# Performance work log

Hardware: AMD Instinct MI355X
Metric: run time of the kernel (lower is better)

Reference implementation:

```python
import jax, jax.numpy as jnp
import numpy as np

LN_EPS = 1e-5


def setup_inputs() -> dict:
    key = jax.random.key(0)
    ks = jax.random.split(key, 6)
    N, E, D = 100000, 600000, 128
    x = jax.random.normal(ks[0], (N, D), dtype=jnp.float32)
    edge_index = jax.random.randint(ks[1], (2, E), 0, N, dtype=jnp.int64)
    dropout_mask = jax.random.uniform(ks[2], (N, D), dtype=jnp.float32)
    ln_gamma = jnp.ones((D,), dtype=jnp.float32)
    ln_beta = jnp.zeros((D,), dtype=jnp.float32)
    W_l = jax.random.normal(ks[3], (D, D), dtype=jnp.float32) / np.sqrt(D)
    b_l = jnp.zeros((D,), dtype=jnp.float32)
    W_r = jax.random.normal(ks[4], (D, D), dtype=jnp.float32) / np.sqrt(D)
    return {"x": x, "edge_index": edge_index, "dropout_mask": dropout_mask,
            "ln_gamma": ln_gamma, "ln_beta": ln_beta,
            "W_l": W_l, "b_l": b_l, "W_r": W_r}


def reference(x, edge_index, dropout_mask, ln_gamma, ln_beta, W_l, b_l, W_r):
    N = x.shape[0]
    # LayerNorm (elementwise affine) -> ReLU -> dropout mask
    mu = jnp.mean(x, axis=-1, keepdims=True)
    var = jnp.mean(jnp.square(x - mu), axis=-1, keepdims=True)
    h = (x - mu) * jax.lax.rsqrt(var + LN_EPS) * ln_gamma + ln_beta
    h = jax.nn.relu(h) * dropout_mask  # [N, D]
    # SAGEConv with mean aggregation: messages flow src -> dst
    src, dst = edge_index[0], edge_index[1]
    agg = jax.ops.segment_sum(h[src], dst, num_segments=N)  # [N, D]
    cnt = jax.ops.segment_sum(jnp.ones_like(dst, dtype=h.dtype), dst,
                              num_segments=N)
    mean_agg = agg / jnp.maximum(cnt, 1.0)[:, None]
    # out = lin_l(mean_agg) + lin_r(h); PyG stores weights as [out, in]
    return mean_agg @ W_l.T + b_l + h @ W_r.T
```

## Files before the change

kernel.cpp:

```cpp
#include <hip/hip_runtime.h>

#define LN_EPS 1e-5f
#define D 128
#define SCAN_CHUNK 1024
#define LDSA_STRIDE 264

typedef __attribute__((ext_vector_type(4))) float f32x4;
typedef __attribute__((ext_vector_type(8))) short bf16x8;

static __device__ __forceinline__ ushort f2bf(float f) {
    union { float f; unsigned u; } a; a.f = f;
    unsigned r = a.u + 0x7FFF + ((a.u >> 16) & 1);
    return (ushort)(r >> 16);
}
static __device__ __forceinline__ float bf2f(ushort u) {
    union { unsigned u; float f; } a; a.u = ((unsigned)u) << 16;
    return a.f;
}

__global__ void prep_w(const float* __restrict__ Wl,
                       const float* __restrict__ Wr,
                       ushort* __restrict__ Bfrag) {
    int t = blockIdx.x * blockDim.x + threadIdx.x;
    if (t >= 8 * 8 * 64 * 8) return;
    int i    = t & 7;
    int lane = (t >> 3) & 63;
    int jb   = (t >> 9) & 7;
    int ks   = t >> 12;
    int k = ks * 32 + (lane >> 4) * 8 + i;
    int j = jb * 16 + (lane & 15);
    float v = (k < D) ? Wl[j * D + k] : Wr[j * D + (k - D)];
    Bfrag[t] = f2bf(v);
}

__global__ void ln_relu_drop(const float* __restrict__ x,
                             const float* __restrict__ mask,
                             const float* __restrict__ gamma,
                             const float* __restrict__ beta,
                             ushort* __restrict__ hbf, int N) {
    int node = (blockIdx.x * blockDim.x + threadIdx.x) >> 6;
    int lane = threadIdx.x & 63;
    if (node >= N) return;
    float2 v = ((const float2*)(x + (size_t)node * D))[lane];
    float s  = v.x + v.y;
    float ss = v.x * v.x + v.y * v.y;
#pragma unroll
    for (int off = 32; off > 0; off >>= 1) {
        s  += __shfl_xor(s, off);
        ss += __shfl_xor(ss, off);
    }
    float mu  = s * (1.0f / D);
    float var = ss * (1.0f / D) - mu * mu;
    float rs  = rsqrtf(var + LN_EPS);
    float2 g = ((const float2*)gamma)[lane];
    float2 b = ((const float2*)beta)[lane];
    float2 m = ((const float2*)(mask + (size_t)node * D))[lane];
    ushort2 o;
    o.x = f2bf(fmaxf((v.x - mu) * rs * g.x + b.x, 0.0f) * m.x);
    o.y = f2bf(fmaxf((v.y - mu) * rs * g.y + b.y, 0.0f) * m.y);
    ((ushort2*)(hbf + (size_t)node * D))[lane] = o;
}

__global__ void hist_k(const int* __restrict__ ei, int* __restrict__ hist, int E) {
    int e = blockIdx.x * blockDim.x + threadIdx.x;
    if (e >= E) return;
    atomicAdd(&hist[ei[E + e]], 1);
}

__global__ void scan1(const int* __restrict__ hist, int* __restrict__ offs,
                      int* __restrict__ chunk_sums, int N) {
    __shared__ int lds[256];
    int base = blockIdx.x * SCAN_CHUNK;
    int t = threadIdx.x;
    int idx0 = base + t * 4;
    int v[4];
#pragma unroll
    for (int i = 0; i < 4; i++) {
        int idx = idx0 + i;
        v[i] = (idx < N) ? hist[idx] : 0;
    }
    lds[t] = v[0] + v[1] + v[2] + v[3];
    __syncthreads();
    for (int off = 1; off < 256; off <<= 1) {
        int add = (t >= off) ? lds[t - off] : 0;
        __syncthreads();
        lds[t] += add;
        __syncthreads();
    }
    int run = (t == 0) ? 0 : lds[t - 1];
    if (t == 255) chunk_sums[blockIdx.x] = lds[255];
#pragma unroll
    for (int i = 0; i < 4; i++) {
        int idx = idx0 + i;
        if (idx < N) offs[idx] = run;
        run += v[i];
    }
}

__global__ void scan2(int* __restrict__ chunk_sums, int C) {
    __shared__ int lds[128];
    int t = threadIdx.x;
    lds[t] = (t < C) ? chunk_sums[t] : 0;
    __syncthreads();
    for (int off = 1; off < 128; off <<= 1) {
        int add = (t >= off) ? lds[t - off] : 0;
        __syncthreads();
        lds[t] += add;
        __syncthreads();
    }
    int excl = (t == 0) ? 0 : lds[t - 1];
    if (t < C) chunk_sums[t] = excl;
}

__global__ void scan3(int* __restrict__ offs, const int* __restrict__ chunk_sums,
                      int* __restrict__ cursor, int N) {
    int i = blockIdx.x * blockDim.x + threadIdx.x;
    if (i >= N) return;
    int v = offs[i] + chunk_sums[i / SCAN_CHUNK];
    offs[i] = v;
    cursor[i] = v;
}

__global__ void sort_edges(const int* __restrict__ ei, int* __restrict__ cursor,
                           int* __restrict__ sorted_src, int E) {
    int e = blockIdx.x * blockDim.x + threadIdx.x;
    if (e >= E) return;
    int dst = ei[E + e];
    int pos = atomicAdd(&cursor[dst], 1);
    sorted_src[pos] = ei[e];
}

__global__ void aggregate4(const ushort* __restrict__ hbf,
                           const int* __restrict__ sorted_src,
                           const int* __restrict__ offs,
                           const int* __restrict__ hist,
                           ushort* __restrict__ magg, int N) {
    int wid  = (blockIdx.x * blockDim.x + threadIdx.x) >> 6;
    int lane = threadIdx.x & 63;
    int g  = lane >> 4;
    int sl = lane & 15;
    int node = wid * 4 + g;
    bool valid = node < N;
    int start = 0, deg = 0;
    if (valid) { start = offs[node]; deg = hist[node]; }
    float acc[8];
#pragma unroll
    for (int j = 0; j < 8; j++) acc[j] = 0.0f;
    for (int i = 0; ; i++) {
        bool act = (i < deg);
        if (!__any(act)) break;
        if (act) {
            int src = sorted_src[start + i];
            bf16x8 v = *(const bf16x8*)(hbf + (size_t)src * D + sl * 8);
#pragma unroll
            for (int j = 0; j < 8; j++) acc[j] += bf2f((ushort)v[j]);
        }
    }
    if (valid) {
        float inv = 1.0f / fmaxf((float)deg, 1.0f);
        bf16x8 o;
#pragma unroll
        for (int j = 0; j < 8; j++) o[j] = (short)f2bf(acc[j] * inv);
        *(bf16x8*)(magg + (size_t)node * D + sl * 8) = o;
    }
}

__global__ void __launch_bounds__(256, 3)
out_gemm_mfma(float* __restrict__ out,
              const ushort* __restrict__ magg,
              const ushort* __restrict__ hbf,
              const ushort* __restrict__ Bfrag,
              const float* __restrict__ bl,
              int N) {
    __shared__ ushort Alds[64 * LDSA_STRIDE];
    int tid  = threadIdx.x;
    int wave = tid >> 6;
    int lane = tid & 63;
    int n0 = blockIdx.x * 64;

    bf16x8 breg[8][2];
#pragma unroll
    for (int ks = 0; ks < 8; ks++)
#pragma unroll
        for (int jj = 0; jj < 2; jj++) {
            int jb = wave * 2 + jj;
            breg[ks][jj] = *(const bf16x8*)(Bfrag + (size_t)((ks * 8 + jb) * 64 + lane) * 8);
        }

#pragma unroll
    for (int it = 0; it < 4; it++) {
        int chunk = tid + 256 * it;
        int row = chunk >> 4;
        int c8  = chunk & 15;
        int node = n0 + row;
        bf16x8 va = (bf16x8){0,0,0,0,0,0,0,0};
        bf16x8 vh = (bf16x8){0,0,0,0,0,0,0,0};
        if (node < N) {
            va = *(const bf16x8*)(magg + (size_t)node * D + c8 * 8);
            vh = *(const bf16x8*)(hbf  + (size_t)node * D + c8 * 8);
        }
        *(bf16x8*)&Alds[row * LDSA_STRIDE + c8 * 8]       = va;
        *(bf16x8*)&Alds[row * LDSA_STRIDE + 128 + c8 * 8] = vh;
    }
    __syncthreads();

    f32x4 acc[4][2];
#pragma unroll
    for (int nb = 0; nb < 4; nb++)
#pragma unroll
        for (int jj = 0; jj < 2; jj++)
            acc[nb][jj] = (f32x4){0.f, 0.f, 0.f, 0.f};

    int arow = lane & 15;
    int akoff = (lane >> 4) * 8;
#pragma unroll
    for (int ks = 0; ks < 8; ks++) {
#pragma unroll
        for (int nb = 0; nb < 4; nb++) {
            bf16x8 a = *(const bf16x8*)&Alds[(nb * 16 + arow) * LDSA_STRIDE + ks * 32 + akoff];
            acc[nb][0] = __builtin_amdgcn_mfma_f32_16x16x32_bf16(a, breg[ks][0], acc[nb][0], 0, 0, 0);
            acc[nb][1] = __builtin_amdgcn_mfma_f32_16x16x32_bf16(a, breg[ks][1], acc[nb][1], 0, 0, 0);
        }
    }

    float bias0 = bl[wave * 32 + (lane & 15)];
    float bias1 = bl[wave * 32 + 16 + (lane & 15)];
    int rbase = (lane >> 4) * 4;
#pragma unroll
    for (int nb = 0; nb < 4; nb++) {
#pragma unroll
        for (int r = 0; r < 4; r++) {
            int row = nb * 16 + rbase + r;
            if (n0 + row < N) {
                float* orow = out + (size_t)(n0 + row) * D + wave * 32 + (lane & 15);
                orow[0]  = acc[nb][0][r] + bias0;
                orow[16] = acc[nb][1][r] + bias1;
            }
        }
    }
}

extern "C" void kernel_launch(void* const* d_in, const int* in_sizes, int n_in,
                              void* d_out, int out_size, void* d_ws, size_t ws_size,
                              hipStream_t stream) {
    const float* x     = (const float*)d_in[0];
    const int*   ei    = (const int*)  d_in[1];
    const float* mask  = (const float*)d_in[2];
    const float* gamma = (const float*)d_in[3];
    const float* beta  = (const float*)d_in[4];
    const float* Wl    = (const float*)d_in[5];
    const float* bl    = (const float*)d_in[6];
    const float* Wr    = (const float*)d_in[7];
    float* out = (float*)d_out;

    int N = in_sizes[0] / D;
    int E = in_sizes[1] / 2;
    int chunks = (N + SCAN_CHUNK - 1) / SCAN_CHUNK;

    ushort* hbf   = (ushort*)d_ws;
    ushort* magg  = hbf + (size_t)N * D;
    ushort* Bfrag = magg + (size_t)N * D;
    int* hist   = (int*)(Bfrag + 32768);
    int* offs   = hist + N;
    int* cursor = offs + N;
    int* csums  = cursor + N;
    int* ssrc   = csums + 128;

    hipMemsetAsync(hist, 0, (size_t)N * sizeof(int), stream);
    prep_w<<<128, 256, 0, stream>>>(Wl, Wr, Bfrag);
    ln_relu_drop<<<(N + 3) / 4, 256, 0, stream>>>(x, mask, gamma, beta, hbf, N);
    hist_k<<<(E + 255) / 256, 256, 0, stream>>>(ei, hist, E);
    scan1<<<chunks, 256, 0, stream>>>(hist, offs, csums, N);
    scan2<<<1, 128, 0, stream>>>(csums, chunks);
    scan3<<<(N + 255) / 256, 256, 0, stream>>>(offs, csums, cursor, N);
    sort_edges<<<(E + 255) / 256, 256, 0, stream>>>(ei, cursor, ssrc, E);
    aggregate4<<<((N + 3) / 4 + 3) / 4, 256, 0, stream>>>(hbf, ssrc, offs, hist, magg, N);
    out_gemm_mfma<<<(N + 63) / 64, 256, 0, stream>>>(out, magg, hbf, Bfrag, bl, N);
}
```

Before: 273.7 us.

## Fuse LN with histogram, merge scan passes, unroll aggregation gather

Histogram blocks are folded into the LayerNorm launch so both run in one grid. The single-block scan2 and scan3 are replaced by one scan_fix kernel in which each block sums the preceding chunk totals itself. The aggregation loop drops its wave-wide __any check and gathers two neighbours per iteration to get more loads in flight. Together these remove two kernel launches and a serial single-block pass, at the cost of some redundant chunk-sum reads and per-lane loop divergence.

```diff
diff --git a/kernel.cpp b/kernel.cpp
--- a/kernel.cpp
+++ b/kernel.cpp
@@ -33,11 +33,19 @@
     Bfrag[t] = f2bf(v);
 }
 
-__global__ void ln_relu_drop(const float* __restrict__ x,
-                             const float* __restrict__ mask,
-                             const float* __restrict__ gamma,
-                             const float* __restrict__ beta,
-                             ushort* __restrict__ hbf, int N) {
+__global__ void ln_hist(const float* __restrict__ x,
+                        const float* __restrict__ mask,
+                        const float* __restrict__ gamma,
+                        const float* __restrict__ beta,
+                        ushort* __restrict__ hbf,
+                        const int* __restrict__ ei,
+                        int* __restrict__ hist,
+                        int N, int E, int lnBlocks) {
+    if (blockIdx.x >= (unsigned)lnBlocks) {
+        int e = (blockIdx.x - lnBlocks) * blockDim.x + threadIdx.x;
+        if (e < E) atomicAdd(&hist[ei[E + e]], 1);
+        return;
+    }
     int node = (blockIdx.x * blockDim.x + threadIdx.x) >> 6;
     int lane = threadIdx.x & 63;
     if (node >= N) return;
@@ -61,12 +69,6 @@
     ((ushort2*)(hbf + (size_t)node * D))[lane] = o;
 }
 
-__global__ void hist_k(const int* __restrict__ ei, int* __restrict__ hist, int E) {
-    int e = blockIdx.x * blockDim.x + threadIdx.x;
-    if (e >= E) return;
-    atomicAdd(&hist[ei[E + e]], 1);
-}
-
 __global__ void scan1(const int* __restrict__ hist, int* __restrict__ offs,
                       int* __restrict__ chunk_sums, int N) {
     __shared__ int lds[256];
@@ -97,26 +99,22 @@
     }
 }
 
-__global__ void scan2(int* __restrict__ chunk_sums, int C) {
-    __shared__ int lds[128];
+__global__ void scan_fix(int* __restrict__ offs, const int* __restrict__ csums,
+                         int* __restrict__ cursor, int N) {
+    __shared__ int base_s;
+    int chunk = (blockIdx.x * 256) / SCAN_CHUNK;
     int t = threadIdx.x;
-    lds[t] = (t < C) ? chunk_sums[t] : 0;
+    if (t < 64) {
+        int v = 0;
+        for (int c = t; c < chunk; c += 64) v += csums[c];
+#pragma unroll
+        for (int off = 32; off > 0; off >>= 1) v += __shfl_xor(v, off);
+        if (t == 0) base_s = v;
+    }
     __syncthreads();
-    for (int off = 1; off < 128; off <<= 1) {
-        int add = (t >= off) ? lds[t - off] : 0;
-        __syncthreads();
-        lds[t] += add;
-        __syncthreads();
-    }
-    int excl = (t == 0) ? 0 : lds[t - 1];
-    if (t < C) chunk_sums[t] = excl;
-}
-
-__global__ void scan3(int* __restrict__ offs, const int* __restrict__ chunk_sums,
-                      int* __restrict__ cursor, int N) {
-    int i = blockIdx.x * blockDim.x + threadIdx.x;
+    int i = blockIdx.x * 256 + t;
     if (i >= N) return;
-    int v = offs[i] + chunk_sums[i / SCAN_CHUNK];
+    int v = offs[i] + base_s;
     offs[i] = v;
     cursor[i] = v;
 }
@@ -146,15 +144,21 @@
     float acc[8];
 #pragma unroll
     for (int j = 0; j < 8; j++) acc[j] = 0.0f;
-    for (int i = 0; ; i++) {
-        bool act = (i < deg);
-        if (!__any(act)) break;
-        if (act) {
-            int src = sorted_src[start + i];
-            bf16x8 v = *(const bf16x8*)(hbf + (size_t)src * D + sl * 8);
-#pragma unroll
-            for (int j = 0; j < 8; j++) acc[j] += bf2f((ushort)v[j]);
-        }
+    int i = 0;
+    for (; i + 2 <= deg; i += 2) {
+        int s0 = sorted_src[start + i];
+        int s1 = sorted_src[start + i + 1];
+        bf16x8 v0 = *(const bf16x8*)(hbf + (size_t)s0 * D + sl * 8);
+        bf16x8 v1 = *(const bf16x8*)(hbf + (size_t)s1 * D + sl * 8);
+#pragma unroll
+        for (int j = 0; j < 8; j++)
+            acc[j] += bf2f((ushort)v0[j]) + bf2f((ushort)v1[j]);
+    }
+    if (i < deg) {
+        int s0 = sorted_src[start + i];
+        bf16x8 v0 = *(const bf16x8*)(hbf + (size_t)s0 * D + sl * 8);
+#pragma unroll
+        for (int j = 0; j < 8; j++) acc[j] += bf2f((ushort)v0[j]);
     }
     if (valid) {
         float inv = 1.0f / fmaxf((float)deg, 1.0f);
@@ -266,13 +270,15 @@
     int* csums  = cursor + N;
     int* ssrc   = csums + 128;
 
+    int lnBlocks = (N + 3) / 4;
+    int histBlocks = (E + 255) / 256;
+
     hipMemsetAsync(hist, 0, (size_t)N * sizeof(int), stream);
     prep_w<<<128, 256, 0, stream>>>(Wl, Wr, Bfrag);
-    ln_relu_drop<<<(N + 3) / 4, 256, 0, stream>>>(x, mask, gamma, beta, hbf, N);
-    hist_k<<<(E + 255) / 256, 256, 0, stream>>>(ei, hist, E);
+    ln_hist<<<lnBlocks + histBlocks, 256, 0, stream>>>(x, mask, gamma, beta, hbf,
+                                                       ei, hist, N, E, lnBlocks);
     scan1<<<chunks, 256, 0, stream>>>(hist, offs, csums, N);
-    scan2<<<1, 128, 0, stream>>>(csums, chunks);
-    scan3<<<(N + 255) / 256, 256, 0, stream>>>(offs, csums, cursor, N);
+    scan_fix<<<(N + 255) / 256, 256, 0, stream>>>(offs, csums, cursor, N);
     sort_edges<<<(E + 255) / 256, 256, 0, stream>>>(ei, cursor, ssrc, E);
     aggregate4<<<((N + 3) / 4 + 3) / 4, 256, 0, stream>>>(hbf, ssrc, offs, hist, magg, N);
     out_gemm_mfma<<<(N + 63) / 64, 256, 0, stream>>>(out, magg, hbf, Bfrag, bl, N);
```

Result: faster. 265.0 us (-3.2%).
